# Performance work log

Hardware: AMD Instinct MI355X
Metric: run time of the kernel (lower is better)

## Reference

```python
import jax, jax.numpy as jnp
import numpy as np

B, C, H, W = 4, 8, 384, 384
NUM_LAYERS = 5
CG_ITERS = 10


def conv2d(x, w, b):
    # x: [B,Cin,H,W], w: [Cout,Cin,3,3]
    y = jax.lax.conv_general_dilated(x, w, (1, 1), 'SAME',
                                     dimension_numbers=('NCHW', 'OIHW', 'NCHW'))
    return y + b[None, :, None, None]


def dw(x, w_in, b_in, ws_mid, bs_mid, w_out, b_out):
    # Sequence: conv, conv, relu, conv, conv, relu, conv, conv, relu, conv, conv, relu, conv
    h = conv2d(x, w_in, b_in)
    for i in range(7):
        h = conv2d(h, ws_mid[i], bs_mid[i])
        if i % 2 == 0:  # ReLU after convs 2,4,6,8
            h = jax.nn.relu(h)
    h = conv2d(h, w_out, b_out)
    return x + h  # residual


def conjugate_grad(rhs, csm_c, mask, lam):
    # rhs: [B,H,W] complex; csm_c: [B,C,H,W] complex; mask: [B,H,W] real
    def AtA(p):
        coil = csm_c * p[:, None]                      # [B,C,H,W]
        k = jnp.fft.fft2(coil) * mask[:, None]         # masked k-space
        return jnp.sum(jnp.conj(csm_c) * jnp.fft.ifft2(k), axis=1)

    def body(carry, _):
        x, r, p, rTr = carry
        Ap = AtA(p) + lam * p
        pAp = jnp.sum(jnp.conj(p) * Ap, axis=(-2, -1)).real
        alpha = rTr / pAp
        x = x + alpha[:, None, None] * p
        r = r - alpha[:, None, None] * Ap
        rTrNew = jnp.sum(jnp.conj(r) * r, axis=(-2, -1)).real
        beta = rTrNew / rTr
        p = r + beta[:, None, None] * p
        return (x, r, p, rTrNew), None

    x0 = jnp.zeros_like(rhs)
    rTr0 = jnp.sum(jnp.conj(rhs) * rhs, axis=(-2, -1)).real
    (x, _, _, _), _ = jax.lax.scan(body, (x0, rhs, rhs, rTr0), None, length=CG_ITERS)
    return x


def reference(under_img, csm, mask, lam, w_in, b_in, ws_mid, bs_mid, w_out, b_out):
    csm_c = jax.lax.complex(csm[..., 0], csm[..., 1])  # [B,C,H,W] complex
    lam_s = lam[0]
    x = under_img
    for _ in range(NUM_LAYERS):
        x = dw(x, w_in, b_in, ws_mid, bs_mid, w_out, b_out)
        x = under_img + lam_s * x
        rhs = jax.lax.complex(x[:, 0], x[:, 1])        # view_as_complex(permute(0,2,3,1))
        xc = conjugate_grad(rhs, csm_c, mask, lam_s)
        x = jnp.stack([xc.real, xc.imag], axis=1)      # view_as_real -> [B,2,H,W]
    return x


def setup_inputs() -> dict:
    key = jax.random.key(0)
    ks = jax.random.split(key, 8)
    under_img = jax.random.normal(ks[0], (B, 2, H, W), jnp.float32)
    csm = jax.random.normal(ks[1], (B, C, H, W, 2), jnp.float32) / np.sqrt(C)
    mask = (jax.random.uniform(ks[2], (B, H, W)) > 0.5).astype(jnp.float32)
    lam = jnp.array([0.05], jnp.float32)
    w_in = jax.random.normal(ks[3], (64, 2, 3, 3), jnp.float32) * 0.02
    b_in = jnp.zeros((64,), jnp.float32)
    ws_mid = jax.random.normal(ks[4], (7, 64, 64, 3, 3), jnp.float32) * 0.02
    bs_mid = jnp.zeros((7, 64), jnp.float32)
    w_out = jax.random.normal(ks[5], (2, 64, 3, 3), jnp.float32) * 0.02
    b_out = jnp.zeros((2,), jnp.float32)
    return {"under_img": under_img, "csm": csm, "mask": mask, "lam": lam,
            "w_in": w_in, "b_in": b_in, "ws_mid": ws_mid, "bs_mid": bs_mid,
            "w_out": w_out, "b_out": b_out}
```

## Files before the change

### kernel.cpp

```cpp
#include <hip/hip_runtime.h>
#include <hip/hip_bf16.h>
#include <math.h>

#define HH 384
#define WW 384
#define HW (HH*WW)
#define BB 4
#define CC 8
#define NLAYERS 5
#define CGITERS 10
#define PI_F 3.14159265358979323846f

typedef __attribute__((ext_vector_type(8))) short short8;
typedef __attribute__((ext_vector_type(4))) float floatx4;

struct cf { float x, y; };
__device__ __forceinline__ cf cadd(cf a, cf b){ cf r; r.x=a.x+b.x; r.y=a.y+b.y; return r; }
__device__ __forceinline__ cf csub(cf a, cf b){ cf r; r.x=a.x-b.x; r.y=a.y-b.y; return r; }
__device__ __forceinline__ cf cmul(cf a, cf b){ cf r; r.x=a.x*b.x - a.y*b.y; r.y=a.x*b.y + a.y*b.x; return r; }
__device__ __forceinline__ cf csqr(cf a){ cf r; r.x = a.x*a.x - a.y*a.y; r.y = 2.f*a.x*a.y; return r; }
__device__ __forceinline__ cf shflxor(cf v, int m){ cf r; r.x = __shfl_xor(v.x, m); r.y = __shfl_xor(v.y, m); return r; }
__device__ __forceinline__ int brev7(int l){ return (int)(__brev((unsigned)l) >> 25); }
__device__ __forceinline__ int padi(int i){ return i + (i >> 3); }

__device__ __forceinline__ void radix3(cf a0, cf a1, cf a2, float s3, cf y[3]) {
  float tx = a1.x + a2.x, ty_ = a1.y + a2.y;
  float ux = a1.x - a2.x, uy = a1.y - a2.y;
  y[0].x = a0.x + tx;              y[0].y = a0.y + ty_;
  y[1].x = a0.x - 0.5f*tx - s3*uy; y[1].y = a0.y - 0.5f*ty_ + s3*ux;
  y[2].x = a0.x - 0.5f*tx + s3*uy; y[2].y = a0.y - 0.5f*ty_ - s3*ux;
}

template<int SIGN>
__device__ __forceinline__ void fft384_wave(int l, const cf v[6], cf uA[3], cf uB[3]) {
  const float s3 = SIGN * 0.8660254037844386f;
  radix3(v[0], v[2], v[4], s3, uA);
  radix3(v[1], v[3], v[5], s3, uB);
  float sA, cA;
  __sincosf(SIGN * (2.0f * PI_F / 384.0f) * (float)l, &sA, &cA);
  cf wA1; wA1.x = cA; wA1.y = sA;
  cf wA2 = csqr(wA1);
  cf w6; w6.x = 0.5f; w6.y = s3;
  cf wB1 = cmul(wA1, w6);
  cf wB2 = csqr(wB1);
  uA[1] = cmul(uA[1], wA1); uA[2] = cmul(uA[2], wA2);
  uB[1] = cmul(uB[1], wB1); uB[2] = cmul(uB[2], wB2);
  cf u = cmul(wA2, wA1);
  #pragma unroll
  for (int k1 = 0; k1 < 3; ++k1) {
    cf a = uA[k1], b = uB[k1];
    uA[k1] = cadd(a, b);
    uB[k1] = cmul(csub(a, b), u);
  }
  #pragma unroll
  for (int h = 32; h >= 1; h >>= 1) {
    u = csqr(u);
    const bool up = (l & h) != 0;
    #pragma unroll
    for (int k1 = 0; k1 < 3; ++k1) {
      cf pa = shflxor(uA[k1], h);
      cf pb = shflxor(uB[k1], h);
      cf na = up ? cmul(csub(uA[k1], pa), u) : cadd(uA[k1], pa);
      cf nb = up ? cmul(csub(uB[k1], pb), u) : cadd(uB[k1], pb);
      uA[k1] = na; uB[k1] = nb;
    }
  }
}


__global__ void repack_mid_k(const float* __restrict__ ws_mid, __hip_bfloat16* __restrict__ wrep) {
  const int idx = blockIdx.x * 256 + threadIdx.x;
  if (idx >= 7*9*64*64) return;
  const int ci = idx & 63, co = (idx >> 6) & 63, tap = (idx >> 12) % 9, i = idx / (9*4096);
  wrep[idx] = __float2bfloat16(ws_mid[(((size_t)i*64 + co)*64 + ci)*9 + tap]);
}

__global__ void __launch_bounds__(256) conv_in_k(const float* __restrict__ xin,
                                                 const float* __restrict__ w,
                                                 const float* __restrict__ bias,
                                                 __hip_bfloat16* __restrict__ out) {
  __shared__ float tile[2][340];
  const int tx = threadIdx.x & 31, ty = threadIdx.x >> 5;
  const int x0 = blockIdx.x * 32, y0 = blockIdx.y * 8, b = blockIdx.z;
  for (int e = threadIdx.x; e < 680; e += 256) {
    int ci = e / 340, rr = e % 340;
    int iy = y0 - 1 + rr / 34, ix = x0 - 1 + rr % 34;
    float v = 0.f;
    if (iy >= 0 && iy < HH && ix >= 0 && ix < WW)
      v = xin[(b*2 + ci)*HW + iy*WW + ix];
    tile[ci][rr] = v;
  }
  __syncthreads();
  float acc[64];
  #pragma unroll
  for (int co = 0; co < 64; ++co) acc[co] = bias[co];
  #pragma unroll
  for (int ci = 0; ci < 2; ++ci) {
    float v0 = tile[ci][ty*34+tx],     v1 = tile[ci][ty*34+tx+1],     v2 = tile[ci][ty*34+tx+2];
    float v3 = tile[ci][(ty+1)*34+tx], v4 = tile[ci][(ty+1)*34+tx+1], v5 = tile[ci][(ty+1)*34+tx+2];
    float v6 = tile[ci][(ty+2)*34+tx], v7 = tile[ci][(ty+2)*34+tx+1], v8 = tile[ci][(ty+2)*34+tx+2];
    #pragma unroll
    for (int co = 0; co < 64; ++co) {
      const float* wp = w + co*18 + ci*9;
      float a = acc[co];
      a = fmaf(v0, wp[0], a); a = fmaf(v1, wp[1], a); a = fmaf(v2, wp[2], a);
      a = fmaf(v3, wp[3], a); a = fmaf(v4, wp[4], a); a = fmaf(v5, wp[5], a);
      a = fmaf(v6, wp[6], a); a = fmaf(v7, wp[7], a); a = fmaf(v8, wp[8], a);
      acc[co] = a;
    }
  }
  const size_t obase = ((size_t)(b*HH + y0 + ty)*WW + (x0 + tx))*64;
  #pragma unroll
  for (int s = 0; s < 8; ++s) {
    uint4 u;
    __hip_bfloat16* hp = (__hip_bfloat16*)&u;
    #pragma unroll
    for (int j = 0; j < 8; ++j) hp[j] = __float2bfloat16(acc[s*8 + j]);
    *(uint4*)(out + obase + s*8) = u;
  }
}

__global__ void __launch_bounds__(256) conv_mid_mfma_k(
    const __hip_bfloat16* __restrict__ in,
    const __hip_bfloat16* __restrict__ wrep,
    const float* __restrict__ bias,
    __hip_bfloat16* __restrict__ out, int relu) {
  __shared__ __hip_bfloat16 atile[10*34*72];
  const int tid = threadIdx.x;
  const int l = tid & 63, wv = tid >> 6;
  const int x0 = blockIdx.x * 32, y0 = blockIdx.y * 8, b = blockIdx.z;

  for (int e = tid; e < 340*8; e += 256) {
    int p = e >> 3, s = e & 7;
    int iy = y0 - 1 + p / 34, ix = x0 - 1 + p % 34;
    uint4 v = make_uint4(0u, 0u, 0u, 0u);
    if (iy >= 0 && iy < HH && ix >= 0 && ix < WW)
      v = *(const uint4*)(in + ((size_t)(b*HH + iy)*WW + ix)*64 + s*8);
    *(uint4*)(&atile[p*72 + s*8]) = v;
  }

  floatx4 acc[4][4];
  #pragma unroll
  for (int mt = 0; mt < 4; ++mt)
    #pragma unroll
    for (int nt = 0; nt < 4; ++nt)
      acc[mt][nt] = (floatx4){0.f, 0.f, 0.f, 0.f};

  const int kseg = l >> 4;
  const int lr = l & 15;

  const __hip_bfloat16* wlane = wrep + lr*64 + kseg*8;
  short8 bf[4][2];
  #pragma unroll
  for (int nt = 0; nt < 4; ++nt) {
    bf[nt][0] = *(const short8*)(wlane + nt*1024);
    bf[nt][1] = *(const short8*)(wlane + nt*1024 + 32);
  }

  __syncthreads();

  #pragma unroll 1
  for (int tap = 0; tap < 9; ++tap) {
    short8 bfn[4][2];
    if (tap < 8) {
      const __hip_bfloat16* wn = wlane + (tap + 1)*4096;
      #pragma unroll
      for (int nt = 0; nt < 4; ++nt) {
        bfn[nt][0] = *(const short8*)(wn + nt*1024);
        bfn[nt][1] = *(const short8*)(wn + nt*1024 + 32);
      }
    }
    const int dy = tap / 3, dx = tap - dy*3;
    short8 af[4][2];
    #pragma unroll
    for (int mt = 0; mt < 4; ++mt) {
      const int ry = 2*wv + (mt >> 1) + dy;
      const int px = (mt & 1)*16 + lr + dx;
      const __hip_bfloat16* ap = &atile[(ry*34 + px)*72 + kseg*8];
      af[mt][0] = *(const short8*)(ap);
      af[mt][1] = *(const short8*)(ap + 32);
    }
    #pragma unroll
    for (int mt = 0; mt < 4; ++mt)
      #pragma unroll
      for (int nt = 0; nt < 4; ++nt) {
        acc[mt][nt] = __builtin_amdgcn_mfma_f32_16x16x32_bf16(af[mt][0], bf[nt][0], acc[mt][nt], 0, 0, 0);
        acc[mt][nt] = __builtin_amdgcn_mfma_f32_16x16x32_bf16(af[mt][1], bf[nt][1], acc[mt][nt], 0, 0, 0);
      }
    if (tap < 8) {
      #pragma unroll
      for (int nt = 0; nt < 4; ++nt) { bf[nt][0] = bfn[nt][0]; bf[nt][1] = bfn[nt][1]; }
    }
  }

  __syncthreads();
  __hip_bfloat16* otile = atile;
  #pragma unroll
  for (int mt = 0; mt < 4; ++mt) {
    const int row = 2*wv + (mt >> 1);
    #pragma unroll
    for (int nt = 0; nt < 4; ++nt) {
      const int ch = nt*16 + lr;
      const float bv = bias[ch];
      #pragma unroll
      for (int rr = 0; rr < 4; ++rr) {
        const int px = (mt & 1)*16 + kseg*4 + rr;
        float v = acc[mt][nt][rr] + bv;
        if (relu) v = fmaxf(v, 0.f);
        otile[(row*32 + px)*72 + ch] = __float2bfloat16(v);
      }
    }
  }
  __syncthreads();
  #pragma unroll
  for (int iter = 0; iter < 8; ++iter) {
    const int p = iter*32 + (tid >> 3), s = tid & 7;
    const int row = p >> 5, px = p & 31;
    uint4 v = *(const uint4*)(&otile[p*72 + s*8]);
    *(uint4*)(out + ((size_t)(b*HH + y0 + row)*WW + (x0 + px))*64 + s*8) = v;
  }
}

__global__ void __launch_bounds__(256) conv_out_k(const __hip_bfloat16* __restrict__ in,
                                                  const float* __restrict__ w,
                                                  const float* __restrict__ bias,
                                                  const float* __restrict__ xcur,
                                                  const float* __restrict__ under,
                                                  const float* __restrict__ lam,
                                                  cf* __restrict__ r, cf* __restrict__ p,
                                                  cf* __restrict__ xc, float* __restrict__ scL) {
  __shared__ __hip_bfloat16 atile[340*72];
  __shared__ float wl[2*64*9];
  __shared__ float wsum[4];
  const int tid = threadIdx.x;
  const int tx = tid & 31, ty = tid >> 5;
  const int x0 = blockIdx.x * 32, y0 = blockIdx.y * 8, b = blockIdx.z;

  for (int e = tid; e < 340*8; e += 256) {
    int pp = e >> 3, s = e & 7;
    int iy = y0 - 1 + pp / 34, ix = x0 - 1 + pp % 34;
    uint4 v = make_uint4(0u, 0u, 0u, 0u);
    if (iy >= 0 && iy < HH && ix >= 0 && ix < WW)
      v = *(const uint4*)(in + ((size_t)(b*HH + iy)*WW + ix)*64 + s*8);
    *(uint4*)(&atile[pp*72 + s*8]) = v;
  }
  for (int e = tid; e < 2*64*9; e += 256) wl[e] = w[e];
  __syncthreads();

  float a0 = bias[0], a1 = bias[1];
  #pragma unroll 1
  for (int tap = 0; tap < 9; ++tap) {
    const int dy = tap / 3, dx = tap - dy*3;
    const __hip_bfloat16* ap = &atile[((ty + dy)*34 + tx + dx)*72];
    #pragma unroll
    for (int s = 0; s < 8; ++s) {
      short8 v8 = *(const short8*)(ap + s*8);
      const __hip_bfloat16* hv = (const __hip_bfloat16*)&v8;
      #pragma unroll
      for (int j = 0; j < 8; ++j) {
        const float f = __bfloat162float(hv[j]);
        a0 = fmaf(f, wl[(s*8 + j)*9 + tap], a0);
        a1 = fmaf(f, wl[(64 + s*8 + j)*9 + tap], a1);
      }
    }
  }
  const float lamv = lam[0];
  const int y = y0 + ty, x = x0 + tx;
  const int idx2 = y*WW + x;
  float xv0 = xcur[b*2*HW + idx2],  xv1 = xcur[b*2*HW + HW + idx2];
  float u0  = under[b*2*HW + idx2], u1  = under[b*2*HW + HW + idx2];
  float r0 = u0 + lamv * (xv0 + a0);
  float r1 = u1 + lamv * (xv1 + a1);
  const int cidx = b*HW + idx2;
  cf vv; vv.x = r0; vv.y = r1;
  r[cidx] = vv; p[cidx] = vv;
  cf zz; zz.x = 0.f; zz.y = 0.f; xc[cidx] = zz;
  float partial = r0*r0 + r1*r1;
  for (int off = 32; off; off >>= 1) partial += __shfl_down(partial, off);
  const int l = tid & 63, wvid = tid >> 6;
  if (l == 0) wsum[wvid] = partial;
  __syncthreads();
  if (tid == 0) atomicAdd(&scL[b], wsum[0]+wsum[1]+wsum[2]+wsum[3]);
}


__global__ void __launch_bounds__(256) pass_a_k(const cf* __restrict__ rold, cf* __restrict__ rnew,
                                                const cf* __restrict__ pold, cf* __restrict__ pnew,
                                                cf* __restrict__ xc, const cf* __restrict__ Ap,
                                                const cf* __restrict__ csm, cf* __restrict__ t,
                                                float* __restrict__ scL, int it) {
  __shared__ cf rowbuf[4][434];
  const int l = threadIdx.x & 63, wv = threadIdx.x >> 6;
  const int y = blockIdx.x * 4 + wv;
  const int c = blockIdx.y, b = blockIdx.z;
  const int rowoff = b*HW + y*WW;
  cf pv[6];
  if (it == 0) {
    #pragma unroll
    for (int m = 0; m < 6; ++m) pv[m] = pold[rowoff + l + 64*m];
  } else {
    const float rtrp  = scL[(it-1)*4 + b];
    const float pApp  = scL[40 + (it-1)*4 + b];
    const float ApApp = scL[80 + (it-1)*4 + b];
    const float alpha = rtrp / pApp;
    const float rtrn  = alpha*alpha*ApApp - rtrp;
    const float beta  = rtrn / rtrp;
    if (blockIdx.x == 0 && c == 0 && threadIdx.x == 0) scL[it*4 + b] = rtrn;
    #pragma unroll
    for (int m = 0; m < 6; ++m) {
      const int idx = rowoff + l + 64*m;
      cf rv = rold[idx];
      cf av = Ap[idx];
      rv.x -= alpha*av.x; rv.y -= alpha*av.y;
      cf po = pold[idx];
      pv[m].x = rv.x + beta*po.x; pv[m].y = rv.y + beta*po.y;
      if (c == 0) {
        rnew[idx] = rv;
        pnew[idx] = pv[m];
        cf xv = xc[idx]; xv.x += alpha*po.x; xv.y += alpha*po.y; xc[idx] = xv;
      }
    }
  }
  const cf* crow = csm + (b*CC + c)*HW + y*WW;
  cf v[6];
  #pragma unroll
  for (int m = 0; m < 6; ++m) v[m] = cmul(crow[l + 64*m], pv[m]);
  cf uA[3], uB[3];
  fft384_wave<-1>(l, v, uA, uB);
  const int R3 = 3 * brev7(l);
  cf* rb = rowbuf[wv];
  #pragma unroll
  for (int k1 = 0; k1 < 3; ++k1) { rb[padi(k1 + R3)] = uA[k1]; rb[padi(k1 + R3 + 3)] = uB[k1]; }
  cf* trow = t + (b*CC + c)*HW + y*WW;
  #pragma unroll
  for (int m = 0; m < 6; ++m) trow[l + 64*m] = rb[padi(l + 64*m)];
}

__global__ void __launch_bounds__(256) pass_b_k(cf* __restrict__ t, const float* __restrict__ mask) {
  __shared__ cf tile[431*9];
  const int b = blockIdx.z, c = blockIdx.y, x0 = blockIdx.x * 8;
  cf* base = t + (b*CC + c)*HW;
  for (int e = threadIdx.x; e < 3072; e += 256) {
    int y = e >> 3, xx = e & 7;
    tile[padi(y)*9 + xx] = base[y*WW + x0 + xx];
  }
  __syncthreads();
  const int l = threadIdx.x & 63, wv = threadIdx.x >> 6;
  const int R3 = 3 * brev7(l);
  for (int rep = 0; rep < 2; ++rep) {
    const int xx = wv*2 + rep, x = x0 + xx;
    cf v[6];
    #pragma unroll
    for (int m = 0; m < 6; ++m) v[m] = tile[padi(l + 64*m)*9 + xx];
    cf uA[3], uB[3];
    fft384_wave<-1>(l, v, uA, uB);
    const float* mrow = mask + b*HW + x;
    #pragma unroll
    for (int k1 = 0; k1 < 3; ++k1) {
      float mA = mrow[(k1 + R3)*WW], mB = mrow[(k1 + R3 + 3)*WW];
      uA[k1].x *= mA; uA[k1].y *= mA; uB[k1].x *= mB; uB[k1].y *= mB;
    }
    __syncthreads();
    #pragma unroll
    for (int k1 = 0; k1 < 3; ++k1) { tile[padi(k1 + R3)*9 + xx] = uA[k1]; tile[padi(k1 + R3 + 3)*9 + xx] = uB[k1]; }
    __syncthreads();
    #pragma unroll
    for (int m = 0; m < 6; ++m) v[m] = tile[padi(l + 64*m)*9 + xx];
    fft384_wave<1>(l, v, uA, uB);
    const float s = 1.0f / 384.0f;
    #pragma unroll
    for (int k1 = 0; k1 < 3; ++k1) {
      uA[k1].x *= s; uA[k1].y *= s; uB[k1].x *= s; uB[k1].y *= s;
      tile[padi(k1 + R3)*9 + xx] = uA[k1]; tile[padi(k1 + R3 + 3)*9 + xx] = uB[k1];
    }
    __syncthreads();
  }
  for (int e = threadIdx.x; e < 3072; e += 256) {
    int y = e >> 3, xx = e & 7;
    base[y*WW + x0 + xx] = tile[padi(y)*9 + xx];
  }
}

__global__ void __launch_bounds__(256) pass_c_k(const cf* __restrict__ t, const cf* __restrict__ csm,
                                                const cf* __restrict__ p, cf* __restrict__ Ap,
                                                const float* __restrict__ lam,
                                                float* __restrict__ scL, int it) {
  __shared__ cf rowbuf[4][434];
  __shared__ cf redbuf[3][384];
  const int l = threadIdx.x & 63, wv = threadIdx.x >> 6;
  const int y = blockIdx.x, b = blockIdx.y;
  const int R3 = 3 * brev7(l);
  cf* rb = rowbuf[wv];
  cf acc[6] = {};
  #pragma unroll 1
  for (int ci = 0; ci < 2; ++ci) {
    const int c = wv*2 + ci;
    const cf* trow = t + (b*CC + c)*HW + y*WW;
    cf v[6];
    #pragma unroll
    for (int m = 0; m < 6; ++m) v[m] = trow[l + 64*m];
    cf uA[3], uB[3];
    fft384_wave<1>(l, v, uA, uB);
    #pragma unroll
    for (int k1 = 0; k1 < 3; ++k1) { rb[padi(k1 + R3)] = uA[k1]; rb[padi(k1 + R3 + 3)] = uB[k1]; }
    const cf* crow = csm + (b*CC + c)*HW + y*WW;
    #pragma unroll
    for (int m = 0; m < 6; ++m) {
      cf cs = crow[l + 64*m];
      cf wz = rb[padi(l + 64*m)];
      acc[m].x += cs.x*wz.x + cs.y*wz.y;
      acc[m].y += cs.x*wz.y - cs.y*wz.x;
    }
  }
  if (wv > 0) {
    #pragma unroll
    for (int m = 0; m < 6; ++m) redbuf[wv - 1][l + 64*m] = acc[m];
  }
  __syncthreads();
  if (wv == 0) {
    #pragma unroll
    for (int m = 0; m < 6; ++m) {
      #pragma unroll
      for (int j = 0; j < 3; ++j) {
        cf o = redbuf[j][l + 64*m];
        acc[m].x += o.x; acc[m].y += o.y;
      }
    }
    const float lamv = lam[0];
    const float sc384 = 1.0f / 384.0f;
    const cf* prow = p + b*HW + y*WW;
    cf* aprow = Ap + b*HW + y*WW;
    float partial = 0.f, partial2 = 0.f;
    #pragma unroll
    for (int m = 0; m < 6; ++m) {
      cf pv = prow[l + 64*m];
      cf ap; ap.x = acc[m].x*sc384 + lamv*pv.x; ap.y = acc[m].y*sc384 + lamv*pv.y;
      aprow[l + 64*m] = ap;
      partial  += pv.x*ap.x + pv.y*ap.y;
      partial2 += ap.x*ap.x + ap.y*ap.y;
    }
    #pragma unroll
    for (int off = 32; off; off >>= 1) {
      partial  += __shfl_down(partial, off);
      partial2 += __shfl_down(partial2, off);
    }
    if (l == 0) {
      atomicAdd(&scL[40 + it*4 + b], partial);
      atomicAdd(&scL[80 + it*4 + b], partial2);
    }
  }
}

__global__ void __launch_bounds__(256) final_x_k(const cf* __restrict__ xc, const cf* __restrict__ p9,
                                                 const float* __restrict__ scL, float* __restrict__ out) {
  const int idx = blockIdx.x * 256 + threadIdx.x;
  const int b = idx / HW;
  const int rem = idx - b*HW;
  const float alpha = scL[(CGITERS-1)*4 + b] / scL[40 + (CGITERS-1)*4 + b];
  cf xv = xc[idx], pv = p9[idx];
  xv.x += alpha*pv.x; xv.y += alpha*pv.y;
  out[b*2*HW + rem] = xv.x;
  out[b*2*HW + HW + rem] = xv.y;
}

__global__ void zero_sc_k(float* sc) {
  for (int i = threadIdx.x; i < NLAYERS*128; i += 256) sc[i] = 0.f;
}

extern "C" void kernel_launch(void* const* d_in, const int* in_sizes, int n_in,
                              void* d_out, int out_size, void* d_ws, size_t ws_size,
                              hipStream_t stream) {
  (void)in_sizes; (void)n_in; (void)out_size; (void)ws_size;
  const float* under  = (const float*)d_in[0];
  const cf*    csm    = (const cf*)d_in[1];
  const float* mask   = (const float*)d_in[2];
  const float* lam    = (const float*)d_in[3];
  const float* w_in   = (const float*)d_in[4];
  const float* b_in   = (const float*)d_in[5];
  const float* ws_mid = (const float*)d_in[6];
  const float* bs_mid = (const float*)d_in[7];
  const float* w_out  = (const float*)d_in[8];
  const float* b_out  = (const float*)d_in[9];
  float* xcur = (float*)d_out;

  char* bws = (char*)d_ws;
  size_t off = 0;
  auto carve = [&](size_t bytes) { char* pp = bws + off; off += (bytes + 255) & ~(size_t)255; return (void*)pp; };
  __hip_bfloat16* actA = (__hip_bfloat16*)carve((size_t)BB*64*HW*2);
  __hip_bfloat16* actB = (__hip_bfloat16*)carve((size_t)BB*64*HW*2);
  cf* t     = (cf*)carve((size_t)BB*CC*HW*8);
  cf* rbuf0 = (cf*)carve((size_t)BB*HW*8);
  cf* rbuf1 = (cf*)carve((size_t)BB*HW*8);
  cf* pbuf0 = (cf*)carve((size_t)BB*HW*8);
  cf* pbuf1 = (cf*)carve((size_t)BB*HW*8);
  cf* xc    = (cf*)carve((size_t)BB*HW*8);
  cf* Ap    = (cf*)carve((size_t)BB*HW*8);
  float* sc = (float*)carve(4096);
  __hip_bfloat16* wrep = (__hip_bfloat16*)carve((size_t)7*9*64*64*2);

  hipMemcpyAsync(xcur, under, (size_t)BB*2*HW*sizeof(float), hipMemcpyDeviceToDevice, stream);

  zero_sc_k<<<1, 256, 0, stream>>>(sc);
  repack_mid_k<<<(7*9*64*64 + 255)/256, 256, 0, stream>>>(ws_mid, wrep);

  dim3 cgrid(WW/32, HH/8, BB);
  dim3 agrid(HH/4, CC, BB);
  dim3 bgrid(WW/8, CC, BB);
  dim3 c2grid(HH, BB);
  const int egrid = BB*HW/256;

  __hip_bfloat16* bufs[2] = { actA, actB };
  cf* rb[2] = { rbuf0, rbuf1 };
  cf* pb[2] = { pbuf0, pbuf1 };

  for (int layer = 0; layer < NLAYERS; ++layer) {
    float* scL = sc + layer*128;
    conv_in_k<<<cgrid, 256, 0, stream>>>(xcur, w_in, b_in, bufs[0]);
    for (int i = 0; i < 7; ++i) {
      conv_mid_mfma_k<<<cgrid, 256, 0, stream>>>(bufs[i & 1], wrep + (size_t)i*9*4096,
                                                 bs_mid + i*64, bufs[(i + 1) & 1], (i % 2 == 0) ? 1 : 0);
    }
    conv_out_k<<<cgrid, 256, 0, stream>>>(bufs[1], w_out, b_out, xcur, under, lam,
                                          rbuf0, pbuf0, xc, scL);
    for (int it = 0; it < CGITERS; ++it) {
      cf* rold = rb[(it + 1) & 1];
      cf* rnew = rb[it & 1];
      cf* pold = pb[(it + 1) & 1];
      cf* pnew = pb[it & 1];
      if (it == 0) { rold = rbuf0; pold = pbuf0; rnew = rbuf0; pnew = pbuf0; }
      pass_a_k<<<agrid, 256, 0, stream>>>(rold, rnew, pold, pnew, xc, Ap, csm, t, scL, it);
      pass_b_k<<<bgrid, 256, 0, stream>>>(t, mask);
      pass_c_k<<<c2grid, 256, 0, stream>>>(t, csm, pnew, Ap, lam, scL, it);
    }
    final_x_k<<<egrid, 256, 0, stream>>>(xc, pb[(CGITERS - 1) & 1], scL, xcur);
  }
}
```

Measured before the change: 9.536 ms.

## Pad activations with zero border, read conv inputs directly, store FFT intermediate in fp16

```diff
diff --git a/kernel.cpp b/kernel.cpp
--- a/kernel.cpp
+++ b/kernel.cpp
@@ -1,10 +1,13 @@
 #include <hip/hip_runtime.h>
 #include <hip/hip_bf16.h>
+#include <hip/hip_fp16.h>
 #include <math.h>
 
 #define HH 384
 #define WW 384
 #define HW (HH*WW)
+#define PH 386
+#define PW 386
 #define BB 4
 #define CC 8
 #define NLAYERS 5
@@ -22,6 +25,8 @@
 __device__ __forceinline__ cf shflxor(cf v, int m){ cf r; r.x = __shfl_xor(v.x, m); r.y = __shfl_xor(v.y, m); return r; }
 __device__ __forceinline__ int brev7(int l){ return (int)(__brev((unsigned)l) >> 25); }
 __device__ __forceinline__ int padi(int i){ return i + (i >> 3); }
+__device__ __forceinline__ cf h2cf(__half2 h){ float2 f = __half22float2(h); cf r; r.x = f.x; r.y = f.y; return r; }
+__device__ __forceinline__ __half2 cf2h(cf v){ return __floats2half2_rn(v.x, v.y); }
 
 __device__ __forceinline__ void radix3(cf a0, cf a1, cf a2, float s3, cf y[3]) {
   float tx = a1.x + a2.x, ty_ = a1.y + a2.y;
@@ -75,6 +80,22 @@
   wrep[idx] = __float2bfloat16(ws_mid[(((size_t)i*64 + co)*64 + ci)*9 + tap]);
 }
 
+__global__ void zero_border_k(__hip_bfloat16* __restrict__ a0, __hip_bfloat16* __restrict__ a1) {
+  const int idx = blockIdx.x * 256 + threadIdx.x;
+  if (idx >= 2*4*1540*8) return;
+  const int s = idx & 7;
+  int e = idx >> 3;
+  const int buf = e / 6160; e -= buf*6160;
+  const int b = e / 1540;  const int i = e - b*1540;
+  int y, x;
+  if (i < 386)       { y = 0;            x = i; }
+  else if (i < 772)  { y = 385;          x = i - 386; }
+  else if (i < 1156) { y = i - 772 + 1;  x = 0; }
+  else               { y = i - 1156 + 1; x = 385; }
+  __hip_bfloat16* p = (buf ? a1 : a0) + ((size_t)(b*PH + y)*PW + x)*64 + s*8;
+  *(uint4*)p = make_uint4(0u, 0u, 0u, 0u);
+}
+
 __global__ void __launch_bounds__(256) conv_in_k(const float* __restrict__ xin,
                                                  const float* __restrict__ w,
                                                  const float* __restrict__ bias,
@@ -109,7 +130,7 @@
       acc[co] = a;
     }
   }
-  const size_t obase = ((size_t)(b*HH + y0 + ty)*WW + (x0 + tx))*64;
+  const size_t obase = ((size_t)(b*PH + y0 + ty + 1)*PW + (x0 + tx + 1))*64;
   #pragma unroll
   for (int s = 0; s < 8; ++s) {
     uint4 u;
@@ -125,19 +146,13 @@
     const __hip_bfloat16* __restrict__ wrep,
     const float* __restrict__ bias,
     __hip_bfloat16* __restrict__ out, int relu) {
-  __shared__ __hip_bfloat16 atile[10*34*72];
+  __shared__ __hip_bfloat16 otile[256*72];
   const int tid = threadIdx.x;
   const int l = tid & 63, wv = tid >> 6;
   const int x0 = blockIdx.x * 32, y0 = blockIdx.y * 8, b = blockIdx.z;
 
-  for (int e = tid; e < 340*8; e += 256) {
-    int p = e >> 3, s = e & 7;
-    int iy = y0 - 1 + p / 34, ix = x0 - 1 + p % 34;
-    uint4 v = make_uint4(0u, 0u, 0u, 0u);
-    if (iy >= 0 && iy < HH && ix >= 0 && ix < WW)
-      v = *(const uint4*)(in + ((size_t)(b*HH + iy)*WW + ix)*64 + s*8);
-    *(uint4*)(&atile[p*72 + s*8]) = v;
-  }
+  const int kseg = l >> 4;
+  const int lr = l & 15;
 
   floatx4 acc[4][4];
   #pragma unroll
@@ -145,9 +160,6 @@
     #pragma unroll
     for (int nt = 0; nt < 4; ++nt)
       acc[mt][nt] = (floatx4){0.f, 0.f, 0.f, 0.f};
-
-  const int kseg = l >> 4;
-  const int lr = l & 15;
 
   const __hip_bfloat16* wlane = wrep + lr*64 + kseg*8;
   short8 bf[4][2];
@@ -157,7 +169,7 @@
     bf[nt][1] = *(const short8*)(wlane + nt*1024 + 32);
   }
 
-  __syncthreads();
+  const __hip_bfloat16* inb = in + ((size_t)(b*PH + y0 + 2*wv)*PW + x0)*64 + kseg*8;
 
   #pragma unroll 1
   for (int tap = 0; tap < 9; ++tap) {
@@ -174,9 +186,7 @@
     short8 af[4][2];
     #pragma unroll
     for (int mt = 0; mt < 4; ++mt) {
-      const int ry = 2*wv + (mt >> 1) + dy;
-      const int px = (mt & 1)*16 + lr + dx;
-      const __hip_bfloat16* ap = &atile[(ry*34 + px)*72 + kseg*8];
+      const __hip_bfloat16* ap = inb + (((mt >> 1) + dy)*PW + (mt & 1)*16 + lr + dx)*64;
       af[mt][0] = *(const short8*)(ap);
       af[mt][1] = *(const short8*)(ap + 32);
     }
@@ -193,8 +203,6 @@
     }
   }
 
-  __syncthreads();
-  __hip_bfloat16* otile = atile;
   #pragma unroll
   for (int mt = 0; mt < 4; ++mt) {
     const int row = 2*wv + (mt >> 1);
@@ -217,7 +225,7 @@
     const int p = iter*32 + (tid >> 3), s = tid & 7;
     const int row = p >> 5, px = p & 31;
     uint4 v = *(const uint4*)(&otile[p*72 + s*8]);
-    *(uint4*)(out + ((size_t)(b*HH + y0 + row)*WW + (x0 + px))*64 + s*8) = v;
+    *(uint4*)(out + ((size_t)(b*PH + y0 + row + 1)*PW + (x0 + px + 1))*64 + s*8) = v;
   }
 }
 
@@ -238,10 +246,7 @@
 
   for (int e = tid; e < 340*8; e += 256) {
     int pp = e >> 3, s = e & 7;
-    int iy = y0 - 1 + pp / 34, ix = x0 - 1 + pp % 34;
-    uint4 v = make_uint4(0u, 0u, 0u, 0u);
-    if (iy >= 0 && iy < HH && ix >= 0 && ix < WW)
-      v = *(const uint4*)(in + ((size_t)(b*HH + iy)*WW + ix)*64 + s*8);
+    uint4 v = *(const uint4*)(in + ((size_t)(b*PH + y0 + pp/34)*PW + (x0 + pp%34))*64 + s*8);
     *(uint4*)(&atile[pp*72 + s*8]) = v;
   }
   for (int e = tid; e < 2*64*9; e += 256) wl[e] = w[e];
@@ -287,7 +292,7 @@
 __global__ void __launch_bounds__(256) pass_a_k(const cf* __restrict__ rold, cf* __restrict__ rnew,
                                                 const cf* __restrict__ pold, cf* __restrict__ pnew,
                                                 cf* __restrict__ xc, const cf* __restrict__ Ap,
-                                                const cf* __restrict__ csm, cf* __restrict__ t,
+                                                const cf* __restrict__ csm, __half2* __restrict__ t,
                                                 float* __restrict__ scL, int it) {
   __shared__ cf rowbuf[4][434];
   const int l = threadIdx.x & 63, wv = threadIdx.x >> 6;
@@ -331,18 +336,18 @@
   cf* rb = rowbuf[wv];
   #pragma unroll
   for (int k1 = 0; k1 < 3; ++k1) { rb[padi(k1 + R3)] = uA[k1]; rb[padi(k1 + R3 + 3)] = uB[k1]; }
-  cf* trow = t + (b*CC + c)*HW + y*WW;
-  #pragma unroll
-  for (int m = 0; m < 6; ++m) trow[l + 64*m] = rb[padi(l + 64*m)];
-}
-
-__global__ void __launch_bounds__(256) pass_b_k(cf* __restrict__ t, const float* __restrict__ mask) {
+  __half2* trow = t + (b*CC + c)*HW + y*WW;
+  #pragma unroll
+  for (int m = 0; m < 6; ++m) trow[l + 64*m] = cf2h(rb[padi(l + 64*m)]);
+}
+
+__global__ void __launch_bounds__(256) pass_b_k(__half2* __restrict__ t, const float* __restrict__ mask) {
   __shared__ cf tile[431*9];
   const int b = blockIdx.z, c = blockIdx.y, x0 = blockIdx.x * 8;
-  cf* base = t + (b*CC + c)*HW;
+  __half2* base = t + (b*CC + c)*HW;
   for (int e = threadIdx.x; e < 3072; e += 256) {
     int y = e >> 3, xx = e & 7;
-    tile[padi(y)*9 + xx] = base[y*WW + x0 + xx];
+    tile[padi(y)*9 + xx] = h2cf(base[y*WW + x0 + xx]);
   }
   __syncthreads();
   const int l = threadIdx.x & 63, wv = threadIdx.x >> 6;
@@ -377,11 +382,11 @@
   }
   for (int e = threadIdx.x; e < 3072; e += 256) {
     int y = e >> 3, xx = e & 7;
-    base[y*WW + x0 + xx] = tile[padi(y)*9 + xx];
-  }
-}
-
-__global__ void __launch_bounds__(256) pass_c_k(const cf* __restrict__ t, const cf* __restrict__ csm,
+    base[y*WW + x0 + xx] = cf2h(tile[padi(y)*9 + xx]);
+  }
+}
+
+__global__ void __launch_bounds__(256) pass_c_k(const __half2* __restrict__ t, const cf* __restrict__ csm,
                                                 const cf* __restrict__ p, cf* __restrict__ Ap,
                                                 const float* __restrict__ lam,
                                                 float* __restrict__ scL, int it) {
@@ -395,10 +400,10 @@
   #pragma unroll 1
   for (int ci = 0; ci < 2; ++ci) {
     const int c = wv*2 + ci;
-    const cf* trow = t + (b*CC + c)*HW + y*WW;
+    const __half2* trow = t + (b*CC + c)*HW + y*WW;
     cf v[6];
     #pragma unroll
-    for (int m = 0; m < 6; ++m) v[m] = trow[l + 64*m];
+    for (int m = 0; m < 6; ++m) v[m] = h2cf(trow[l + 64*m]);
     cf uA[3], uB[3];
     fft384_wave<1>(l, v, uA, uB);
     #pragma unroll
@@ -486,9 +491,9 @@
   char* bws = (char*)d_ws;
   size_t off = 0;
   auto carve = [&](size_t bytes) { char* pp = bws + off; off += (bytes + 255) & ~(size_t)255; return (void*)pp; };
-  __hip_bfloat16* actA = (__hip_bfloat16*)carve((size_t)BB*64*HW*2);
-  __hip_bfloat16* actB = (__hip_bfloat16*)carve((size_t)BB*64*HW*2);
-  cf* t     = (cf*)carve((size_t)BB*CC*HW*8);
+  __hip_bfloat16* actA = (__hip_bfloat16*)carve((size_t)BB*PH*PW*64*2);
+  __hip_bfloat16* actB = (__hip_bfloat16*)carve((size_t)BB*PH*PW*64*2);
+  __half2* t = (__half2*)carve((size_t)BB*CC*HW*4);
   cf* rbuf0 = (cf*)carve((size_t)BB*HW*8);
   cf* rbuf1 = (cf*)carve((size_t)BB*HW*8);
   cf* pbuf0 = (cf*)carve((size_t)BB*HW*8);
@@ -501,6 +506,7 @@
   hipMemcpyAsync(xcur, under, (size_t)BB*2*HW*sizeof(float), hipMemcpyDeviceToDevice, stream);
 
   zero_sc_k<<<1, 256, 0, stream>>>(sc);
+  zero_border_k<<<(2*4*1540*8 + 255)/256, 256, 0, stream>>>(actA, actB);
   repack_mid_k<<<(7*9*64*64 + 255)/256, 256, 0, stream>>>(ws_mid, wrep);
 
   dim3 cgrid(WW/32, HH/8, BB);
```

Measured after the change: 10.87 ms. 1.14x slower.
